# Kernel tuning notes

Hardware: AMD Instinct MI355X
Metric: run time of the kernel (lower is better)

Reference implementation:

```python
import jax, jax.numpy as jnp
import numpy as np
from functools import partial

M_HEADS, N_LEVELS, N_POINTS = 4, 3, 4


def conv2d(x, w, b, padding=1, dilation=1):
    y = jax.lax.conv_general_dilated(
        x, w, window_strides=(1, 1),
        padding=[(padding, padding), (padding, padding)],
        rhs_dilation=(dilation, dilation),
        dimension_numbers=('NCHW', 'OIHW', 'NCHW'))
    return y + b[None, :, None, None]


def lrelu(x):
    return jnp.where(x >= 0, x, 0.1 * x)


def _bilinear(img, gx, gy, zero_pad):
    # img: (C,H,W); gx,gy: arbitrary shape of pixel coordinates
    C, H, W = img.shape
    x0 = jnp.floor(gx); y0 = jnp.floor(gy)
    wx = gx - x0; wy = gy - y0
    def g(xi, yi):
        xc = jnp.clip(xi, 0, W - 1).astype(jnp.int32)
        yc = jnp.clip(yi, 0, H - 1).astype(jnp.int32)
        v = img[:, yc, xc]  # (C, ...)
        if zero_pad:
            ok = ((xi >= 0) & (xi <= W - 1) & (yi >= 0) & (yi <= H - 1)).astype(img.dtype)
            v = v * ok
        return v
    return (g(x0, y0) * ((1 - wx) * (1 - wy)) + g(x0 + 1, y0) * (wx * (1 - wy))
            + g(x0, y0 + 1) * ((1 - wx) * wy) + g(x0 + 1, y0 + 1) * (wx * wy))


def warp(x, flo):
    # torch grid_sample(padding_mode='border', align_corners=True) at coords grid+flow
    B, C, H, W = x.shape
    yy, xx = jnp.meshgrid(jnp.arange(H, dtype=x.dtype), jnp.arange(W, dtype=x.dtype), indexing='ij')
    gx = xx[None] + flo[:, 0]
    gy = yy[None] + flo[:, 1]
    return jax.vmap(partial(_bilinear, zero_pad=False))(x, gx, gy)


def _forward(frame, srcframe, flow_forward, flow_backward,
             emb_qk_w, emb_qk_b, emb_v_w, emb_v_b, so_w, so_b, aw_w, aw_b,
             vp_w, vp_b, op_w, op_b, ff_w, ff_b, ffn1_w, ffn1_b, ffn2_w, ffn2_b,
             fus_w, fus_b):
    M, L, P = M_HEADS, N_LEVELS, N_POINTS
    b, t, c, h, w = frame.shape
    HW = h * w
    D = c // M
    # flow-warped neighbor frames -> query embedding
    warp01 = warp(frame[:, 0], flow_backward[:, 0])
    warp21 = warp(frame[:, 2], flow_forward[:, 1])
    q_in = jnp.concatenate([warp01, frame[:, 1], warp21, flow_forward[:, 1], flow_backward[:, 0]], axis=1)
    query = lrelu(conv2d(q_in, emb_qk_w, emb_qk_b))  # (b, 3c, h, w)
    value = lrelu(conv2d(frame.reshape(b, t * c, h, w), emb_v_w, emb_v_b)).reshape(b, t, c, h, w)
    # MSDeformAttn_Fusion
    v = conv2d(value.reshape(b * t, c, h, w), vp_w, vp_b).reshape(b, t, c, h, w)  # value_proj per frame
    off = conv2d(query, so_w, so_b)   # (b, M*L*P*2, h, w)
    aw = conv2d(query, aw_w, aw_b)    # (b, M*L*P,   h, w)
    off = off.reshape(b, M * L * P * 2, HW).transpose(0, 2, 1).reshape(b, HW, M, L, P, 2)
    attn = aw.reshape(b, M * L * P, HW).transpose(0, 2, 1).reshape(b, HW, M, L * P)
    attn = jax.nn.softmax(attn, axis=-1).reshape(b, HW, M, L, P)
    # flow-guided offsets: [flow_backward10, 0, flow_forward12] per level
    flow_stack = jnp.stack([flow_backward[:, 0], jnp.zeros_like(flow_forward[:, 1]), flow_forward[:, 1]], axis=2)  # (b,2,L,h,w)
    off = off + flow_stack.reshape(b, 2, L, HW).transpose(0, 3, 2, 1)[:, :, None, :, None, :]
    # normalized reference points (valid ratios are all ones)
    ys, xs = jnp.meshgrid(jnp.arange(h, dtype=frame.dtype) + 0.5,
                          jnp.arange(w, dtype=frame.dtype) + 0.5, indexing='ij')
    ref = jnp.stack([xs.reshape(-1) / w, ys.reshape(-1) / h], axis=-1)  # (HW, 2)
    norm = jnp.array([w, h], dtype=frame.dtype)
    loc = ref[None, :, None, None, None, :] + off / norm  # (b,HW,M,L,P,2) in [0,1]
    # deformable gather: grid_sample(mode=bilinear, padding=zeros, align_corners=False)
    imgs = v.reshape(b, L, M, D, h, w).transpose(0, 2, 1, 3, 4, 5).reshape(b * M * L, D, h, w)
    locs = loc.transpose(0, 2, 3, 1, 4, 5).reshape(b * M * L, HW, P, 2)
    gx = locs[..., 0] * w - 0.5   # align_corners=False pixel coords
    gy = locs[..., 1] * h - 0.5
    sampled = jax.vmap(partial(_bilinear, zero_pad=True))(imgs, gx, gy)  # (b*M*L, D, HW, P)
    sampled = sampled.reshape(b, M, L, D, HW, P)
    out = jnp.einsum('nmldqp,nqmlp->nqmd', sampled, attn).reshape(b, HW, c)
    out = out.reshape(b, h, w, c).transpose(0, 3, 1, 2)
    out = conv2d(out, op_w, op_b)  # output_proj
    # post-attention feed-forward + fusion
    out = conv2d(out, ff_w, ff_b) + frame[:, 1]
    ffn = lrelu(conv2d(jnp.concatenate([out, srcframe[:, 1]], axis=1), ffn1_w, ffn1_b, padding=2, dilation=2))
    out = out + conv2d(ffn, ffn2_w, ffn2_b)
    out = lrelu(conv2d(out, fus_w, fus_b, padding=0))
    return out


def setup_inputs() -> dict:
    key = jax.random.key(0)
    ks = jax.random.split(key, 28)
    b, t, c, h, w = 2, 3, 32, 256, 256
    M, L, P = M_HEADS, N_LEVELS, N_POINTS
    def rn(k, shape, s=1.0):
        return jax.random.normal(k, shape, dtype=jnp.float32) * s
    return {
        'frame': rn(ks[0], (b, t, c, h, w)),
        'srcframe': rn(ks[1], (b, t, c, h, w)),
        'flow_forward': rn(ks[2], (b, 2, 2, h, w), 2.0),
        'flow_backward': rn(ks[3], (b, 2, 2, h, w), 2.0),
        'emb_qk_w': rn(ks[4], (3 * c, 3 * c + 4, 3, 3), 0.05), 'emb_qk_b': rn(ks[5], (3 * c,), 0.02),
        'emb_v_w': rn(ks[6], (3 * c, 3 * c, 3, 3), 0.05), 'emb_v_b': rn(ks[7], (3 * c,), 0.02),
        'so_w': rn(ks[8], (M * L * P * 2, 3 * c, 3, 3), 0.01), 'so_b': rn(ks[9], (M * L * P * 2,), 0.5),
        'aw_w': rn(ks[10], (M * L * P, 3 * c, 3, 3), 0.05), 'aw_b': rn(ks[11], (M * L * P,), 0.02),
        'vp_w': rn(ks[12], (c, c, 3, 3), 0.05), 'vp_b': rn(ks[13], (c,), 0.02),
        'op_w': rn(ks[14], (c, c, 3, 3), 0.05), 'op_b': rn(ks[15], (c,), 0.02),
        'ff_w': rn(ks[16], (c, c, 3, 3), 0.05), 'ff_b': rn(ks[17], (c,), 0.02),
        'ffn1_w': rn(ks[18], (c, 2 * c, 3, 3), 0.05), 'ffn1_b': rn(ks[19], (c,), 0.02),
        'ffn2_w': rn(ks[20], (c, c, 3, 3), 0.05), 'ffn2_b': rn(ks[21], (c,), 0.02),
        'fus_w': rn(ks[22], (c, c, 1, 1), 0.05), 'fus_b': rn(ks[23], (c,), 0.02),
    }


def reference(frame, srcframe, flow_forward, flow_backward,
              emb_qk_w, emb_qk_b, emb_v_w, emb_v_b, so_w, so_b, aw_w, aw_b,
              vp_w, vp_b, op_w, op_b, ff_w, ff_b, ffn1_w, ffn1_b, ffn2_w, ffn2_b,
              fus_w, fus_b):
    return _forward(frame, srcframe, flow_forward, flow_backward,
                    emb_qk_w, emb_qk_b, emb_v_w, emb_v_b, so_w, so_b, aw_w, aw_b,
                    vp_w, vp_b, op_w, op_b, ff_w, ff_b, ffn1_w, ffn1_b, ffn2_w, ffn2_b,
                    fus_w, fus_b)
```

## Files before the change

### kernel.cpp

```cpp
#include <hip/hip_runtime.h>
#include <cmath>

typedef _Float16 half_t;
typedef _Float16 half8 __attribute__((ext_vector_type(8)));
typedef _Float16 half4 __attribute__((ext_vector_type(4)));
typedef float floatx4 __attribute__((ext_vector_type(4)));

__device__ __forceinline__ float lrelu_f(float v) { return v >= 0.f ? v : 0.1f * v; }

template <int CIN, int COTOT>
__device__ __forceinline__ void pack_one(const float* __restrict__ w,
                                         half_t* __restrict__ o,
                                         int co_off, int co_n, int i)
{
    constexpr int NCB = (CIN + 31) / 32;
    int ci = i & 31;
    int t = i >> 5;
    int col = t % co_n; t /= co_n;
    int cb = t % NCB;
    int tap = t / NCB;
    int cg = cb * 32 + ci;
    float v = (cg < CIN) ? w[((long)col * CIN + cg) * 9 + tap] : 0.f;
    o[(((long)tap * NCB + cb) * COTOT + co_off + col) * 32 + ci] = (half_t)v;
}

__global__ __launch_bounds__(256) void prep_w_all(
    const float* __restrict__ qk, const float* __restrict__ ev,
    const float* __restrict__ so, const float* __restrict__ aw,
    const float* __restrict__ vp, const float* __restrict__ op,
    const float* __restrict__ ffw, const float* __restrict__ f1,
    const float* __restrict__ f2,
    half_t* wq, half_t* wv, half_t* wsoaw, half_t* wvp2, half_t* wop2,
    half_t* wff2, half_t* wffn1, half_t* wffn2)
{
    int i = blockIdx.x * 256 + threadIdx.x;
    constexpr int C0 = 110592;
    constexpr int C1 = C0 + 82944;
    constexpr int C2 = C1 + 82944;
    constexpr int C3 = C2 + 41472;
    constexpr int C4 = C3 + 9216;
    constexpr int C5 = C4 + 9216;
    constexpr int C6 = C5 + 9216;
    constexpr int C7 = C6 + 18432;
    constexpr int C8 = C7 + 9216;
    if (i < C0)      pack_one<100, 96>(qk, wq, 0, 96, i);
    else if (i < C1) pack_one<96, 96>(ev, wv, 0, 96, i - C0);
    else if (i < C2) pack_one<96, 144>(so, wsoaw, 0, 96, i - C1);
    else if (i < C3) pack_one<96, 144>(aw, wsoaw, 96, 48, i - C2);
    else if (i < C4) pack_one<32, 32>(vp, wvp2, 0, 32, i - C3);
    else if (i < C5) pack_one<32, 32>(op, wop2, 0, 32, i - C4);
    else if (i < C6) pack_one<32, 32>(ffw, wff2, 0, 32, i - C5);
    else if (i < C7) pack_one<64, 32>(f1, wffn1, 0, 32, i - C6);
    else if (i < C8) pack_one<32, 32>(f2, wffn2, 0, 32, i - C7);
}

__global__ __launch_bounds__(256) void copy_cl_kernel(
    const float* __restrict__ frame, const float* __restrict__ srcframe,
    const float* __restrict__ ff, const float* __restrict__ fb,
    half_t* __restrict__ qin, half_t* __restrict__ fcl,
    half_t* __restrict__ o3rec, int H, int W)
{
    const int HW = H * W;
    const int p = threadIdx.x >> 2, sub = threadIdx.x & 3;
    const int q = blockIdx.x * 64 + p;
    const int b = blockIdx.y;
    const long fbase = (long)b * 96 * HW;
    const long rq = ((long)b * HW + q) * 112;
    const long rf = ((long)b * HW + q) * 96;
    const long r3 = ((long)b * HW + q) * 64;

    half8 c0, c2;
    #pragma unroll
    for (int d = 0; d < 8; ++d) {
        c0[d] = (half_t)frame[fbase + (long)(sub * 8 + d) * HW + q];
        c2[d] = (half_t)frame[fbase + (long)(64 + sub * 8 + d) * HW + q];
    }
    *(half8*)&fcl[rf + sub * 8] = c0;
    *(half8*)&fcl[rf + 64 + sub * 8] = c2;

    half8 fv, sv;
    #pragma unroll
    for (int d = 0; d < 8; ++d) {
        long off = fbase + (long)(32 + sub * 8 + d) * HW + q;
        fv[d] = (half_t)frame[off];
        sv[d] = (half_t)srcframe[off];
    }
    *(half8*)&qin[rq + 32 + sub * 8] = fv;
    *(half8*)&fcl[rf + 32 + sub * 8] = fv;
    *(half8*)&o3rec[r3 + 32 + sub * 8] = sv;

    if (sub == 0) {
        half8 fl = {};
        fl[0] = (half_t)ff[((long)(b * 2 + 1) * 2 + 0) * HW + q];
        fl[1] = (half_t)ff[((long)(b * 2 + 1) * 2 + 1) * HW + q];
        fl[2] = (half_t)fb[((long)(b * 2 + 0) * 2 + 0) * HW + q];
        fl[3] = (half_t)fb[((long)(b * 2 + 0) * 2 + 1) * HW + q];
        *(half8*)&qin[rq + 96] = fl;
    } else if (sub == 1) {
        half8 z = {};
        *(half8*)&qin[rq + 104] = z;
    }
}

__global__ __launch_bounds__(256) void warp_cl_kernel(
    const half_t* __restrict__ fcl, const float* __restrict__ ff,
    const float* __restrict__ fb, half_t* __restrict__ qin, int H, int W)
{
    const int HW = H * W;
    const int p = threadIdx.x >> 2, sub = threadIdx.x & 3;
    const int q = blockIdx.x * 64 + p;
    const int b = blockIdx.y;
    const int x = q % W, y = q / W;
    const long rq = ((long)b * HW + q) * 112;
    const half_t* fc = fcl + (long)b * HW * 96;

    const float fb0x = fb[((long)(b * 2 + 0) * 2 + 0) * HW + q];
    const float fb0y = fb[((long)(b * 2 + 0) * 2 + 1) * HW + q];
    const float ff1x = ff[((long)(b * 2 + 1) * 2 + 0) * HW + q];
    const float ff1y = ff[((long)(b * 2 + 1) * 2 + 1) * HW + q];

    #pragma unroll
    for (int t = 0; t < 2; ++t) {
        const float fx = t ? ff1x : fb0x;
        const float fy = t ? ff1y : fb0y;
        const int coff = t ? 64 : 0;
        float gx = (float)x + fx, gy = (float)y + fy;
        float x0f = floorf(gx), y0f = floorf(gy);
        float wx = gx - x0f, wy = gy - y0f;
        int x0 = min(max((int)x0f, 0), W - 1);
        int x1 = min(max((int)x0f + 1, 0), W - 1);
        int y0 = min(max((int)y0f, 0), H - 1);
        int y1 = min(max((int)y0f + 1, 0), H - 1);
        float w00 = (1.f - wx) * (1.f - wy), w10 = wx * (1.f - wy);
        float w01 = (1.f - wx) * wy, w11 = wx * wy;

        half8 v00 = *(const half8*)&fc[(long)(y0 * W + x0) * 96 + coff + sub * 8];
        half8 v10 = *(const half8*)&fc[(long)(y0 * W + x1) * 96 + coff + sub * 8];
        half8 v01 = *(const half8*)&fc[(long)(y1 * W + x0) * 96 + coff + sub * 8];
        half8 v11 = *(const half8*)&fc[(long)(y1 * W + x1) * 96 + coff + sub * 8];

        half8 st;
        #pragma unroll
        for (int d = 0; d < 8; ++d) {
            float v = (float)v00[d] * w00 + (float)v10[d] * w10 +
                      (float)v01[d] * w01 + (float)v11[d] * w11;
            st[d] = (half_t)v;
        }
        *(half8*)&qin[rq + coff + sub * 8] = st;
    }
}

template <int CREC, int CIN, int COUT, int DIL, bool LRELU, int RESID_MODE,
          int OUTC, int SPLIT, bool OUT_TGROUP, int RESREC>
__global__ __launch_bounds__(512, 2) void conv3x3_cl(
    const half_t* __restrict__ in, long in_stride,
    const half_t* __restrict__ w16,
    const float* __restrict__ bias0, const float* __restrict__ bias1,
    const void* __restrict__ resid, long resid_stride,
    half_t* __restrict__ out, long out_stride, int H, int W)
{
    constexpr int NCB = (CIN + 31) / 32;
    constexpr int S = 16 + 2 * DIL;
    constexpr int NF = COUT / 16;
    constexpr int COPAD = COUT + 2;
    constexpr int NLD = S * S * 4;
    constexpr int NITEM = (NLD + 511) / 512;
    constexpr int WCH = 9 * 4 * COPAD;
    constexpr int NWIT = (WCH + 511) / 512;
    __shared__ half_t sa[32 * S * S];
    __shared__ half_t sw[WCH * 8];

    const int n = blockIdx.y;
    const int tile = blockIdx.x;
    const int tx = tile & 15, ty = tile >> 4;
    const int tid = threadIdx.x;
    const int wv = tid >> 6, lane = tid & 63;
    const int cl = lane & 15, jk = lane >> 4;

    floatx4 acc[2][NF] = {};

    const int gy0 = ty * 16 - DIL, gx0 = tx * 16 - DIL;
    const int HWl = H * W;
    const half_t* ib = in + (long)n * in_stride;

    int pxv[NITEM], gofs[NITEM];
    bool inb[NITEM];
    #pragma unroll
    for (int k = 0; k < NITEM; ++k) {
        int i = tid + k * 512;
        int pix = i >> 2;
        int sy = pix / S, sx = pix - sy * S;
        int gy = gy0 + sy, gx = gx0 + sx;
        pxv[k] = pix;
        inb[k] = (i < NLD) && gy >= 0 && gy < H && gx >= 0 && gx < W;
        gofs[k] = gy * W + gx;
    }

    half8 ra[NITEM], rw[NWIT];
    auto LOADA = [&](int cb) {
        #pragma unroll
        for (int k = 0; k < NITEM; ++k) {
            int i = tid + k * 512;
            int c_g = cb * 4 + (i & 3);
            half8 v = {};
            if (inb[k] && (c_g * 8 + 8 <= CREC))
                v = *(const half8*)&ib[(long)gofs[k] * CREC + c_g * 8];
            ra[k] = v;
        }
    };
    auto WRITEA = [&]() {
        #pragma unroll
        for (int k = 0; k < NITEM; ++k) {
            int i = tid + k * 512;
            if (i < NLD) {
                int pix = pxv[k], chunk = i & 3;
                *(half8*)&sa[((pix << 2) + (chunk ^ ((pix >> 1) & 3))) << 3] = ra[k];
            }
        }
    };
    auto LOADW = [&](int cb) {
        #pragma unroll
        for (int k = 0; k < NWIT; ++k) {
            int j = tid + k * 512;
            int tj = j / COPAD;
            int co = j - tj * COPAD;
            half8 v = {};
            if (j < WCH && co < COUT) {
                int tap = tj >> 2, jj = tj & 3;
                v = *(const half8*)&w16[(((long)tap * NCB + cb) * COUT + co) * 32 + jj * 8];
            }
            rw[k] = v;
        }
    };
    auto WRITEW = [&]() {
        #pragma unroll
        for (int k = 0; k < NWIT; ++k) {
            int j = tid + k * 512;
            if (j < WCH) *(half8*)&sw[j * 8] = rw[k];
        }
    };

    LOADA(0); LOADW(0);
    WRITEA(); WRITEW();
    __syncthreads();

    for (int cb = 0; cb < NCB; ++cb) {
        if (cb + 1 < NCB) { LOADA(cb + 1); LOADW(cb + 1); }

        #pragma unroll
        for (int tap = 0; tap < 9; ++tap) {
            const int ky = tap / 3, kx = tap % 3;
            half8 af[2];
            #pragma unroll
            for (int m = 0; m < 2; ++m) {
                int pix = (wv * 2 + m + ky * DIL) * S + kx * DIL + cl;
                af[m] = *(const half8*)&sa[((pix << 2) + (jk ^ ((pix >> 1) & 3))) << 3];
            }
            const int wbase = ((tap << 2) | jk) * COPAD + cl;
            #pragma unroll
            for (int nn = 0; nn < NF; ++nn) {
                half8 bf = *(const half8*)&sw[(wbase + nn * 16) * 8];
                acc[0][nn] = __builtin_amdgcn_mfma_f32_16x16x32_f16(af[0], bf, acc[0][nn], 0, 0, 0);
                acc[1][nn] = __builtin_amdgcn_mfma_f32_16x16x32_f16(af[1], bf, acc[1][nn], 0, 0, 0);
            }
        }

        if (cb + 1 < NCB) {
            __syncthreads();
            WRITEA(); WRITEW();
            __syncthreads();
        }
    }

    const int x0 = tx * 16 + jk * 4;
    #pragma unroll
    for (int m = 0; m < 2; ++m) {
        const int yy = ty * 16 + wv * 2 + m;
        #pragma unroll
        for (int nn = 0; nn < NF; ++nn) {
            const int co = nn * 16 + cl;
            float bv = (co < SPLIT) ? bias0[co] : bias1[co - SPLIT];
            float r[4];
            #pragma unroll
            for (int i = 0; i < 4; ++i) r[i] = acc[m][nn][i] + bv;
            if constexpr (RESID_MODE == 1) {
                const float* rp = (const float*)resid + (long)n * resid_stride +
                                  (long)co * HWl + (long)yy * W + x0;
                float4 rv = *(const float4*)rp;
                r[0] += rv.x; r[1] += rv.y; r[2] += rv.z; r[3] += rv.w;
            } else if constexpr (RESID_MODE == 3) {
                const half_t* rp = (const half_t*)resid +
                                   ((long)n * HWl + (long)yy * W + x0) * RESREC + co;
                #pragma unroll
                for (int i = 0; i < 4; ++i) r[i] += (float)rp[i * RESREC];
            }
            if (LRELU) {
                #pragma unroll
                for (int i = 0; i < 4; ++i) r[i] = lrelu_f(r[i]);
            }
            if constexpr (OUT_TGROUP) {
                long base = ((long)(n * 3 + (co >> 5)) * HWl + (long)yy * W + x0) * 32 + (co & 31);
                #pragma unroll
                for (int i = 0; i < 4; ++i) out[base + i * 32] = (half_t)r[i];
            } else {
                long base = (long)n * out_stride + ((long)yy * W + x0) * OUTC + co;
                #pragma unroll
                for (int i = 0; i < 4; ++i) out[base + i * OUTC] = (half_t)r[i];
            }
        }
    }
}

__global__ __launch_bounds__(256) void deform_v2(
    const half_t* __restrict__ v_cl, const half_t* __restrict__ offaw,
    const float* __restrict__ ff, const float* __restrict__ fb,
    half_t* __restrict__ out1, int H, int W)
{
    const int HW = H * W;
    const int bid = blockIdx.x;
    const int swz = (bid & 7) * 32 + (bid >> 3);
    const int tx = swz & 15, ty = swz >> 4;
    const int b = blockIdx.y;
    const int r = threadIdx.x >> 4, c = threadIdx.x & 15;
    const int x = tx * 16 + c, y = ty * 16 + r;
    const int q = y * W + x;

    const half8* rec8 = (const half8*)&offaw[((long)b * HW + q) * 144];
    half8 rec[18];
    #pragma unroll
    for (int i = 0; i < 18; ++i) rec[i] = rec8[i];

    float fbx = fb[((long)(b * 2 + 0) * 2 + 0) * HW + q];
    float fby = fb[((long)(b * 2 + 0) * 2 + 1) * HW + q];
    float ffx = ff[((long)(b * 2 + 1) * 2 + 0) * HW + q];
    float ffy = ff[((long)(b * 2 + 1) * 2 + 1) * HW + q];

    float o[32];
    #pragma unroll
    for (int i = 0; i < 32; ++i) o[i] = 0.f;

    #pragma unroll
    for (int m = 0; m < 4; ++m) {
        float a[12], mx = -1e30f;
        #pragma unroll
        for (int i = 0; i < 12; ++i) {
            int ii = 96 + m * 12 + i;
            a[i] = (float)rec[ii >> 3][ii & 7];
            mx = fmaxf(mx, a[i]);
        }
        float s = 0.f;
        #pragma unroll
        for (int i = 0; i < 12; ++i) { a[i] = expf(a[i] - mx); s += a[i]; }
        float inv = 1.f / s;

        #pragma unroll
        for (int l = 0; l < 3; ++l) {
            float fx = (l == 0) ? fbx : (l == 2) ? ffx : 0.f;
            float fy = (l == 0) ? fby : (l == 2) ? ffy : 0.f;
            const half_t* img = v_cl + (long)(b * 3 + l) * HW * 32 + m * 8;
            #pragma unroll
            for (int p = 0; p < 4; ++p) {
                int oc = ((m * 3 + l) * 4 + p) * 2;
                float gx = (float)x + (float)rec[oc >> 3][oc & 7] + fx;
                float gy = (float)y + (float)rec[(oc + 1) >> 3][(oc + 1) & 7] + fy;
                float wgt = a[l * 4 + p] * inv;
                float x0f = floorf(gx), y0f = floorf(gy);
                float wx = gx - x0f, wy = gy - y0f;
                int x0 = (int)x0f, y0 = (int)y0f;
                #pragma unroll
                for (int t_ = 0; t_ < 4; ++t_) {
                    int xi = x0 + (t_ & 1), yi = y0 + (t_ >> 1);
                    float wt = ((t_ & 1) ? wx : 1.f - wx) *
                               ((t_ >> 1) ? wy : 1.f - wy) * wgt;
                    if (xi >= 0 && xi < W && yi >= 0 && yi < H) {
                        const half8 vv = *(const half8*)&img[(long)(yi * W + xi) * 32];
                        #pragma unroll
                        for (int d = 0; d < 8; ++d)
                            o[m * 8 + d] = fmaf(wt, (float)vv[d], o[m * 8 + d]);
                    }
                }
            }
        }
    }
    #pragma unroll
    for (int ch = 0; ch < 4; ++ch) {
        half8 st;
        #pragma unroll
        for (int d = 0; d < 8; ++d) st[d] = (half_t)o[ch * 8 + d];
        *(half8*)&out1[((long)b * HW + q) * 32 + ch * 8] = st;
    }
}

__global__ __launch_bounds__(256) void conv1x1_f16(
    const half_t* __restrict__ in, const float* __restrict__ w,
    const float* __restrict__ bias, float* __restrict__ out, int HW)
{
    int q = blockIdx.x * 256 + threadIdx.x;
    if (q >= HW) return;
    long b = blockIdx.y;
    const half8* ip = (const half8*)&in[((long)b * HW + q) * 32];
    half8 vv[4];
    #pragma unroll
    for (int i = 0; i < 4; ++i) vv[i] = ip[i];
    float v[32];
    #pragma unroll
    for (int ci = 0; ci < 32; ++ci) v[ci] = (float)vv[ci >> 3][ci & 7];
    float* ob = out + b * 32 * HW;
    #pragma unroll
    for (int co = 0; co < 32; ++co) {
        float acc = bias[co];
        #pragma unroll
        for (int ci = 0; ci < 32; ++ci) acc = fmaf(w[co * 32 + ci], v[ci], acc);
        ob[(long)co * HW + q] = lrelu_f(acc);
    }
}

extern "C" void kernel_launch(void* const* d_in, const int* in_sizes, int n_in,
                              void* d_out, int out_size, void* d_ws, size_t ws_size,
                              hipStream_t stream)
{
    (void)in_sizes; (void)n_in; (void)out_size; (void)ws_size;
    const int H = 256, W = 256, HW = H * W, B = 2;

    const float* frame    = (const float*)d_in[0];
    const float* srcframe = (const float*)d_in[1];
    const float* ff       = (const float*)d_in[2];
    const float* fb       = (const float*)d_in[3];
    const float* emb_qk_w = (const float*)d_in[4];
    const float* emb_qk_b = (const float*)d_in[5];
    const float* emb_v_w  = (const float*)d_in[6];
    const float* emb_v_b  = (const float*)d_in[7];
    const float* so_w     = (const float*)d_in[8];
    const float* so_b     = (const float*)d_in[9];
    const float* aw_w     = (const float*)d_in[10];
    const float* aw_b     = (const float*)d_in[11];
    const float* vp_w     = (const float*)d_in[12];
    const float* vp_b     = (const float*)d_in[13];
    const float* op_w     = (const float*)d_in[14];
    const float* op_b     = (const float*)d_in[15];
    const float* ff_w     = (const float*)d_in[16];
    const float* ff_b     = (const float*)d_in[17];
    const float* ffn1_w   = (const float*)d_in[18];
    const float* ffn1_b   = (const float*)d_in[19];
    const float* ffn2_w   = (const float*)d_in[20];
    const float* ffn2_b   = (const float*)d_in[21];
    const float* fus_w    = (const float*)d_in[22];
    const float* fus_b    = (const float*)d_in[23];

    half_t* hw = (half_t*)d_ws;
    half_t* q_in_cl = hw;
    half_t* fcl     = hw + 14680064L;
    half_t* value_g = hw + 27262976L;
    half_t* offaw   = hw + 14680064L;
    half_t* query_c = hw + 39845888L;
    half_t* v_cl    = hw + 52428800L;
    half_t* out1    = hw + 65011712L;
    half_t* out2    = hw + 69206016L;
    half_t* o3rec   = hw + 73400320L;
    half_t* ffnb    = hw + 81788928L;
    half_t* out4    = hw + 85983232L;
    half_t* wq      = hw + 90177536L;
    half_t* wv      = hw + 90288128L;
    half_t* wsoaw   = hw + 90371072L;
    half_t* wvp     = hw + 90495488L;
    half_t* wop     = hw + 90504704L;
    half_t* wff     = hw + 90513920L;
    half_t* wffn1   = hw + 90523136L;
    half_t* wffn2   = hw + 90541568L;

    dim3 blk(256);
    dim3 cblk(512);
    dim3 convGrid(256, B);

    prep_w_all<<<(373248 + 255) / 256, blk, 0, stream>>>(
        emb_qk_w, emb_v_w, so_w, aw_w, vp_w, op_w, ff_w, ffn1_w, ffn2_w,
        wq, wv, wsoaw, wvp, wop, wff, wffn1, wffn2);

    copy_cl_kernel<<<dim3(HW / 64, B), blk, 0, stream>>>(frame, srcframe, ff, fb,
                                                         q_in_cl, fcl, o3rec, H, W);
    warp_cl_kernel<<<dim3(HW / 64, B), blk, 0, stream>>>(fcl, ff, fb, q_in_cl, H, W);

    conv3x3_cl<112, 100, 96, 1, true, 0, 96, 96, false, 0>
        <<<convGrid, cblk, 0, stream>>>(q_in_cl, (long)HW * 112, wq, emb_qk_b, nullptr,
                                        nullptr, 0, query_c, (long)HW * 96, H, W);
    conv3x3_cl<96, 96, 96, 1, true, 0, 32, 96, true, 0>
        <<<convGrid, cblk, 0, stream>>>(fcl, (long)HW * 96, wv, emb_v_b, nullptr,
                                        nullptr, 0, value_g, 0, H, W);
    conv3x3_cl<32, 32, 32, 1, false, 0, 32, 32, false, 0>
        <<<dim3(256, 6), cblk, 0, stream>>>(value_g, (long)HW * 32, wvp, vp_b, nullptr,
                                            nullptr, 0, v_cl, (long)HW * 32, H, W);
    conv3x3_cl<96, 96, 144, 1, false, 0, 144, 96, false, 0>
        <<<convGrid, cblk, 0, stream>>>(query_c, (long)HW * 96, wsoaw, so_b, aw_b,
                                        nullptr, 0, offaw, (long)HW * 144, H, W);
    deform_v2<<<dim3(256, B), blk, 0, stream>>>(v_cl, offaw, ff, fb, out1, H, W);
    conv3x3_cl<32, 32, 32, 1, false, 0, 32, 32, false, 0>
        <<<convGrid, cblk, 0, stream>>>(out1, (long)HW * 32, wop, op_b, nullptr,
                                        nullptr, 0, out2, (long)HW * 32, H, W);
    conv3x3_cl<32, 32, 32, 1, false, 1, 64, 32, false, 0>
        <<<convGrid, cblk, 0, stream>>>(out2, (long)HW * 32, wff, ff_b, nullptr,
                                        frame + 32L * HW, 96L * HW, o3rec, (long)HW * 64, H, W);
    conv3x3_cl<64, 64, 32, 2, true, 0, 32, 32, false, 0>
        <<<convGrid, cblk, 0, stream>>>(o3rec, (long)HW * 64, wffn1, ffn1_b, nullptr,
                                        nullptr, 0, ffnb, (long)HW * 32, H, W);
    conv3x3_cl<32, 32, 32, 1, false, 3, 32, 32, false, 64>
        <<<convGrid, cblk, 0, stream>>>(ffnb, (long)HW * 32, wffn2, ffn2_b, nullptr,
                                        o3rec, 0, out4, (long)HW * 32, H, W);
    conv1x1_f16<<<dim3(HW / 256, B), blk, 0, stream>>>(out4, fus_w, fus_b,
                                                       (float*)d_out, HW);
}
```

Measured before the change: 308.9 us.

## Split deformable attention across heads with one thread per pixel-head pair

The deformable sampling kernel now assigns four threads per query pixel, one per attention head, instead of one thread doing all four heads. Blocks cover 8x8 pixel tiles and the grid grows fourfold. Each thread loads only its head's offsets and weights and keeps 8 accumulators instead of 32. This is meant to cut register pressure, raise occupancy and give more parallel gather latency hiding, at the cost of redundant flow loads and more threads overall.

```diff
diff --git a/kernel.cpp b/kernel.cpp
--- a/kernel.cpp
+++ b/kernel.cpp
@@ -311,84 +311,77 @@
     }
 }
 
-__global__ __launch_bounds__(256) void deform_v2(
+__global__ __launch_bounds__(256) void deform_v3(
     const half_t* __restrict__ v_cl, const half_t* __restrict__ offaw,
     const float* __restrict__ ff, const float* __restrict__ fb,
     half_t* __restrict__ out1, int H, int W)
 {
     const int HW = H * W;
     const int bid = blockIdx.x;
-    const int swz = (bid & 7) * 32 + (bid >> 3);
-    const int tx = swz & 15, ty = swz >> 4;
+    const int swz = (bid & 7) * 128 + (bid >> 3);
+    const int tx = swz & 31, ty = swz >> 5;
     const int b = blockIdx.y;
-    const int r = threadIdx.x >> 4, c = threadIdx.x & 15;
-    const int x = tx * 16 + c, y = ty * 16 + r;
+    const int p = threadIdx.x >> 2;
+    const int m = threadIdx.x & 3;
+    const int x = tx * 8 + (p & 7), y = ty * 8 + (p >> 3);
     const int q = y * W + x;
 
-    const half8* rec8 = (const half8*)&offaw[((long)b * HW + q) * 144];
-    half8 rec[18];
-    #pragma unroll
-    for (int i = 0; i < 18; ++i) rec[i] = rec8[i];
+    const half_t* rec = &offaw[((long)b * HW + q) * 144];
+    half8 offv[3];
+    #pragma unroll
+    for (int i = 0; i < 3; ++i) offv[i] = *(const half8*)&rec[m * 24 + i * 8];
+    half4 awv[3];
+    #pragma unroll
+    for (int i = 0; i < 3; ++i) awv[i] = *(const half4*)&rec[96 + m * 12 + i * 4];
 
     float fbx = fb[((long)(b * 2 + 0) * 2 + 0) * HW + q];
     float fby = fb[((long)(b * 2 + 0) * 2 + 1) * HW + q];
     float ffx = ff[((long)(b * 2 + 1) * 2 + 0) * HW + q];
     float ffy = ff[((long)(b * 2 + 1) * 2 + 1) * HW + q];
 
-    float o[32];
-    #pragma unroll
-    for (int i = 0; i < 32; ++i) o[i] = 0.f;
-
-    #pragma unroll
-    for (int m = 0; m < 4; ++m) {
-        float a[12], mx = -1e30f;
-        #pragma unroll
-        for (int i = 0; i < 12; ++i) {
-            int ii = 96 + m * 12 + i;
-            a[i] = (float)rec[ii >> 3][ii & 7];
-            mx = fmaxf(mx, a[i]);
-        }
-        float s = 0.f;
-        #pragma unroll
-        for (int i = 0; i < 12; ++i) { a[i] = expf(a[i] - mx); s += a[i]; }
-        float inv = 1.f / s;
-
-        #pragma unroll
-        for (int l = 0; l < 3; ++l) {
-            float fx = (l == 0) ? fbx : (l == 2) ? ffx : 0.f;
-            float fy = (l == 0) ? fby : (l == 2) ? ffy : 0.f;
-            const half_t* img = v_cl + (long)(b * 3 + l) * HW * 32 + m * 8;
+    float a[12], mx = -1e30f;
+    #pragma unroll
+    for (int i = 0; i < 12; ++i) {
+        a[i] = (float)awv[i >> 2][i & 3];
+        mx = fmaxf(mx, a[i]);
+    }
+    float s = 0.f;
+    #pragma unroll
+    for (int i = 0; i < 12; ++i) { a[i] = expf(a[i] - mx); s += a[i]; }
+    float inv = 1.f / s;
+
+    float o[8] = {0, 0, 0, 0, 0, 0, 0, 0};
+    #pragma unroll
+    for (int l = 0; l < 3; ++l) {
+        float fx = (l == 0) ? fbx : (l == 2) ? ffx : 0.f;
+        float fy = (l == 0) ? fby : (l == 2) ? ffy : 0.f;
+        const half_t* img = v_cl + (long)(b * 3 + l) * HW * 32 + m * 8;
+        #pragma unroll
+        for (int pp = 0; pp < 4; ++pp) {
+            int oc = (l * 4 + pp) * 2;
+            float gx = (float)x + (float)offv[oc >> 3][oc & 7] + fx;
+            float gy = (float)y + (float)offv[(oc + 1) >> 3][(oc + 1) & 7] + fy;
+            float wgt = a[l * 4 + pp] * inv;
+            float x0f = floorf(gx), y0f = floorf(gy);
+            float wx = gx - x0f, wy = gy - y0f;
+            int x0 = (int)x0f, y0 = (int)y0f;
             #pragma unroll
-            for (int p = 0; p < 4; ++p) {
-                int oc = ((m * 3 + l) * 4 + p) * 2;
-                float gx = (float)x + (float)rec[oc >> 3][oc & 7] + fx;
-                float gy = (float)y + (float)rec[(oc + 1) >> 3][(oc + 1) & 7] + fy;
-                float wgt = a[l * 4 + p] * inv;
-                float x0f = floorf(gx), y0f = floorf(gy);
-                float wx = gx - x0f, wy = gy - y0f;
-                int x0 = (int)x0f, y0 = (int)y0f;
-                #pragma unroll
-                for (int t_ = 0; t_ < 4; ++t_) {
-                    int xi = x0 + (t_ & 1), yi = y0 + (t_ >> 1);
-                    float wt = ((t_ & 1) ? wx : 1.f - wx) *
-                               ((t_ >> 1) ? wy : 1.f - wy) * wgt;
-                    if (xi >= 0 && xi < W && yi >= 0 && yi < H) {
-                        const half8 vv = *(const half8*)&img[(long)(yi * W + xi) * 32];
-                        #pragma unroll
-                        for (int d = 0; d < 8; ++d)
-                            o[m * 8 + d] = fmaf(wt, (float)vv[d], o[m * 8 + d]);
-                    }
+            for (int t_ = 0; t_ < 4; ++t_) {
+                int xi = x0 + (t_ & 1), yi = y0 + (t_ >> 1);
+                float wt = ((t_ & 1) ? wx : 1.f - wx) *
+                           ((t_ >> 1) ? wy : 1.f - wy) * wgt;
+                if (xi >= 0 && xi < W && yi >= 0 && yi < H) {
+                    const half8 vv = *(const half8*)&img[(long)(yi * W + xi) * 32];
+                    #pragma unroll
+                    for (int d = 0; d < 8; ++d) o[d] = fmaf(wt, (float)vv[d], o[d]);
                 }
             }
         }
     }
-    #pragma unroll
-    for (int ch = 0; ch < 4; ++ch) {
-        half8 st;
-        #pragma unroll
-        for (int d = 0; d < 8; ++d) st[d] = (half_t)o[ch * 8 + d];
-        *(half8*)&out1[((long)b * HW + q) * 32 + ch * 8] = st;
-    }
+    half8 st;
+    #pragma unroll
+    for (int d = 0; d < 8; ++d) st[d] = (half_t)o[d];
+    *(half8*)&out1[((long)b * HW + q) * 32 + m * 8] = st;
 }
 
 __global__ __launch_bounds__(256) void conv1x1_f16(
@@ -492,7 +485,7 @@
     conv3x3_cl<96, 96, 144, 1, false, 0, 144, 96, false, 0>
         <<<convGrid, cblk, 0, stream>>>(query_c, (long)HW * 96, wsoaw, so_b, aw_b,
                                         nullptr, 0, offaw, (long)HW * 144, H, W);
-    deform_v2<<<dim3(256, B), blk, 0, stream>>>(v_cl, offaw, ff, fb, out1, H, W);
+    deform_v3<<<dim3(1024, B), blk, 0, stream>>>(v_cl, offaw, ff, fb, out1, H, W);
     conv3x3_cl<32, 32, 32, 1, false, 0, 32, 32, false, 0>
         <<<convGrid, cblk, 0, stream>>>(out1, (long)HW * 32, wop, op_b, nullptr,
                                         nullptr, 0, out2, (long)HW * 32, H, W);
```

Measured after the change: 274.0 us. 1.13x faster.
